# Kernel tuning notes

Measured on AMD Instinct MI355X. Metric: run time of the kernel, lower is better.

The kernel has to match this reference:

```python
import jax, jax.numpy as jnp
import numpy as np

EMBED_DIM = 256; N_HEADS = 8; HEAD_DIM = 32; N_PAIRS = 16
POS_DIM = 2; N_LEVELS = 4; NBH = [3, 5, 7, 9]
N_Q = 2048; BATCH = 2; FULL = 128
SPATIAL_THETA = 100.0; LEVEL_THETA = 10.0
LN_EPS = 1e-5


def _grids():
    offs, lvls = [], []
    for l, s in enumerate(NBH):
        ax = np.arange(s)
        g = np.stack(np.meshgrid(ax, ax, indexing='ij'), -1).reshape(-1, 2)
        offs.append(g - (s - 1) // 2)
        lvls.append(np.full(s * s, l))
    return (np.concatenate(offs).astype(np.int32), np.concatenate(lvls).astype(np.int32))

OFFSETS, LEVEL_IDS = _grids()  # [164,2], [164]
K_PER_Q = OFFSETS.shape[0]


def _apply_rope(x, pos, freqs):
    # x: [..., n_heads, n_pairs, 2]; pos: [..., 3]; freqs: [3, n_pairs]
    ang = pos @ freqs                      # [..., n_pairs]
    c = jnp.cos(ang)[..., None, :]         # broadcast over heads
    s = jnp.sin(ang)[..., None, :]
    x1, x2 = x[..., 0], x[..., 1]
    return jnp.stack([x1 * c - x2 * s, x1 * s + x2 * c], axis=-1)


def setup_inputs() -> dict:
    key = jax.random.key(0)
    ks = jax.random.split(key, 8)
    scale = EMBED_DIM ** -0.5
    i = jnp.arange(N_PAIRS, dtype=jnp.float32) / N_PAIRS
    rope_freqs = jnp.stack([SPATIAL_THETA ** -i, SPATIAL_THETA ** -i, LEVEL_THETA ** -i])  # [3,16]
    level_spatial_shapes = jnp.array([[FULL >> l, FULL >> l] for l in range(N_LEVELS)], jnp.int32)
    return {
        'query': jax.random.normal(ks[0], (N_Q, EMBED_DIM), jnp.float32),
        'query_spatial_positions': jax.random.uniform(ks[1], (N_Q, POS_DIM), jnp.float32) * (FULL - 1),
        'stacked_feature_maps': jax.random.normal(ks[2], (BATCH, N_LEVELS, FULL, FULL, EMBED_DIM), jnp.float32) * 0.02,
        'norm_w': jnp.ones((EMBED_DIM,), jnp.float32),
        'norm_b': jnp.zeros((EMBED_DIM,), jnp.float32),
        'q_w': jax.random.normal(ks[3], (EMBED_DIM, EMBED_DIM), jnp.float32) * scale,
        'k_w': jax.random.normal(ks[4], (EMBED_DIM, EMBED_DIM), jnp.float32) * scale,
        'v_w': jax.random.normal(ks[5], (EMBED_DIM, EMBED_DIM), jnp.float32) * scale,
        'out_w': jax.random.normal(ks[6], (EMBED_DIM, EMBED_DIM), jnp.float32) * scale,
        'rope_freqs': rope_freqs,
        'query_batch_offsets': jnp.array([0, N_Q // 2, N_Q], jnp.int32),
        'level_spatial_shapes': level_spatial_shapes,
    }


def reference(query, query_spatial_positions, stacked_feature_maps, norm_w, norm_b,
              q_w, k_w, v_w, out_w, rope_freqs, query_batch_offsets, level_spatial_shapes):
    n_q = query.shape[0]
    residual = query

    # pre-LayerNorm
    mu = query.mean(-1, keepdims=True)
    var = query.var(-1, keepdims=True)
    x = (query - mu) * jax.lax.rsqrt(var + LN_EPS) * norm_w + norm_b

    # query projection + RoPE (spatial dims + level dim; queries sit at max-res level 0)
    q = x @ q_w
    qpos = jnp.concatenate([query_spatial_positions, jnp.zeros((n_q, 1), query.dtype)], -1)  # [n_q,3]
    q_rot = _apply_rope(q.reshape(n_q, N_HEADS, N_PAIRS, 2), qpos, rope_freqs).reshape(n_q, N_HEADS, HEAD_DIM)

    # multilevel neighborhood indices
    shapes_f = level_spatial_shapes.astype(query.dtype)               # [L,2]
    scaling = shapes_f / shapes_f.max(0)                              # [L,2]
    scaled = query_spatial_positions[:, None, :] * scaling[None]      # [n_q,L,2]
    centers = jnp.floor(scaled).astype(jnp.int32)                     # [n_q,L,2]
    lvl = jnp.asarray(LEVEL_IDS)                                      # [K]
    idx = centers[:, lvl, :] + jnp.asarray(OFFSETS)[None]             # [n_q,K,2]
    lsh = level_spatial_shapes[lvl]                                   # [K,2]
    valid = jnp.all((idx >= 0) & (idx < lsh[None]), -1)               # [n_q,K]
    idxc = jnp.clip(idx, 0, lsh[None] - 1)

    # per-query batch ids from offsets
    b = jnp.searchsorted(query_batch_offsets, jnp.arange(n_q, dtype=query_batch_offsets.dtype), side='right') - 1

    # sparse gather of key/value features (unspecified -> zero)
    feats = stacked_feature_maps[b[:, None], lvl[None, :], idxc[..., 0], idxc[..., 1]]  # [n_q,K,E]
    feats = feats * valid[..., None].astype(feats.dtype)

    k = feats @ k_w
    v = feats @ v_w

    # key positions at full scale + level coordinate
    stride = (shapes_f.max(0)[None] / shapes_f)[lvl]                  # [K,2]
    kpos_sp = (idx.astype(query.dtype) + 0.5) * stride[None]          # [n_q,K,2]
    kpos = jnp.concatenate([kpos_sp, jnp.broadcast_to(lvl.astype(query.dtype), (n_q, K_PER_Q))[..., None]], -1)
    k_rot = _apply_rope(k.reshape(n_q, K_PER_Q, N_HEADS, N_PAIRS, 2), kpos, rope_freqs)
    k_rot = k_rot.reshape(n_q, K_PER_Q, N_HEADS, HEAD_DIM)

    # attention over the 164 gathered keys per query
    logits = jnp.einsum('nhd,nkhd->nhk', q_rot, k_rot) / np.sqrt(HEAD_DIM)
    logits = jnp.where(valid[:, None, :], logits, jnp.asarray(-1e9, logits.dtype))
    attn = jax.nn.softmax(logits, axis=-1)
    out = jnp.einsum('nhk,nkhd->nhd', attn, v.reshape(n_q, K_PER_Q, N_HEADS, HEAD_DIM))
    out = out.reshape(n_q, EMBED_DIM) @ out_w
    return out + residual
```

## Files before the change

### kernel.cpp

```cpp
#include <hip/hip_runtime.h>
#include <hip/hip_bf16.h>

typedef unsigned short u16;
typedef short short8 __attribute__((ext_vector_type(8)));
typedef float f32x4 __attribute__((ext_vector_type(4)));

#define ROWS_PER_BATCH 21760
#define TOT_ROWS 43520
#define KV_BLOCKS (TOT_ROWS / 128)

__device__ __forceinline__ u16 f2bf(float f){
  unsigned u = __builtin_bit_cast(unsigned, f);
  u += 0x7FFFu + ((u >> 16) & 1u);
  return (u16)(u >> 16);
}
__device__ __forceinline__ float bf2f(u16 h){
  return __builtin_bit_cast(float, ((unsigned)h) << 16);
}
__device__ __forceinline__ float bflo(unsigned u){ return __builtin_bit_cast(float, u << 16); }
__device__ __forceinline__ float bfhi(unsigned u){ return __builtin_bit_cast(float, u & 0xFFFF0000u); }
__device__ __forceinline__ unsigned pk2bf(float a, float b){
  __hip_bfloat162 h = __float22bfloat162_rn(make_float2(a, b));
  union { __hip_bfloat162 h2; unsigned u; } cv; cv.h2 = h; return cv.u;
}

__global__ __launch_bounds__(256) void prep_kernel(
    const float* __restrict__ qw, const float* __restrict__ kw,
    const float* __restrict__ vw, const float* __restrict__ ow,
    const float* __restrict__ q, const float* __restrict__ nw,
    const float* __restrict__ nb,
    u16* __restrict__ wtq, u16* __restrict__ wtk,
    u16* __restrict__ wtv, u16* __restrict__ wto, u16* __restrict__ x){
  const int bx = blockIdx.x;
  const int t = threadIdx.x;
  if (bx < 128){
    int e = bx * 256 + t;
    int which = e >> 13;
    int r = e & 8191;
    int cg = r >> 9;
    int kk = (r >> 6) & 7;
    int lane = r & 63;
    int quad = lane >> 4, mn = lane & 15;
    const float* s = which == 0 ? qw : which == 1 ? kw : which == 2 ? vw : ow;
    u16* d       = which == 0 ? wtq : which == 1 ? wtk : which == 2 ? wtv : wto;
    const float* base = s + (kk * 32 + quad * 8) * 256 + cg * 16 + mn;
    float e8[8];
    #pragma unroll
    for (int j = 0; j < 8; ++j) e8[j] = base[j * 256];
    uint4 o = { pk2bf(e8[0], e8[1]), pk2bf(e8[2], e8[3]),
                pk2bf(e8[4], e8[5]), pk2bf(e8[6], e8[7]) };
    *(uint4*)(d + (size_t)r * 8) = o;
  } else {
    const int row = (bx - 128) * 4 + (t >> 6);
    const int lane = t & 63;
    const float4 v = *(const float4*)(q + (size_t)row * 256 + lane * 4);
    float s1 = v.x + v.y + v.z + v.w;
    float s2 = v.x*v.x + v.y*v.y + v.z*v.z + v.w*v.w;
    #pragma unroll
    for (int o = 32; o > 0; o >>= 1){
      s1 += __shfl_xor(s1, o);
      s2 += __shfl_xor(s2, o);
    }
    float mu = s1 * (1.0f / 256.0f);
    float var = s2 * (1.0f / 256.0f) - mu * mu;
    float rs = rsqrtf(var + 1e-5f);
    const float4 wv = *(const float4*)(nw + lane * 4);
    const float4 bv = *(const float4*)(nb + lane * 4);
    float o0 = (v.x - mu) * rs * wv.x + bv.x;
    float o1 = (v.y - mu) * rs * wv.y + bv.y;
    float o2 = (v.z - mu) * rs * wv.z + bv.z;
    float o3 = (v.w - mu) * rs * wv.w + bv.w;
    uint2 pk = { pk2bf(o0, o1), pk2bf(o2, o3) };
    *(uint2*)(x + (size_t)row * 256 + lane * 4) = pk;
  }
}

__global__ __launch_bounds__(512, 4) void kv_qproj(const float* __restrict__ fm,
        const u16* __restrict__ wtkp, const u16* __restrict__ wtvp,
        const u16* __restrict__ wtqp, const u16* __restrict__ xbf,
        const float* __restrict__ rope,
        u16* __restrict__ krot, u16* __restrict__ vmap,
        float* __restrict__ qraw){
  __shared__ u16 bstage[32 * 512];
  __shared__ float slab[8][16][66];
  __shared__ unsigned sh_cs[8][16][16];

  const int t = threadIdx.x;

  if (blockIdx.x >= KV_BLOCKS){
    const int ob = (blockIdx.x - KV_BLOCKS) * 2 + (t >> 8);
    const int bx = ob & 127, by = ob >> 7;
    const int tt = t & 255;
    const int wv = tt >> 6;
    const int lane = tt & 63;
    const int mn = lane & 15;
    const int quad = lane >> 4;
    const int cg = by * 4 + wv;
    const int row0 = bx * 16;

    short8 af[8];
    {
      const u16* arow = xbf + (size_t)(row0 + mn) * 256 + quad * 8;
      #pragma unroll
      for (int kk = 0; kk < 8; ++kk)
        af[kk] = *(const short8*)(arow + kk * 32);
    }
    const u16* wb = wtqp + (size_t)((cg * 8) * 64 + lane) * 8;
    short8 bc = *(const short8*)wb;
    f32x4 acc = (f32x4){0.f, 0.f, 0.f, 0.f};
    #pragma unroll
    for (int kk = 0; kk < 8; ++kk){
      short8 bn;
      if (kk < 7) bn = *(const short8*)(wb + (size_t)(kk + 1) * 64 * 8);
      acc = __builtin_amdgcn_mfma_f32_16x16x32_bf16(af[kk], bc, acc, 0, 0, 0);
      bc = bn;
    }
    const int col = cg * 16 + mn;
    #pragma unroll
    for (int r = 0; r < 4; ++r)
      qraw[(size_t)(row0 + quad * 4 + r) * 256 + col] = acc[r];
    return;
  }

  const int w = t >> 6;
  const int lane = t & 63;
  const int row0 = blockIdx.x * 128 + w * 16;

  const int b = row0 / ROWS_PER_BATCH;
  const int rr = row0 - b * ROWS_PER_BATCH;
  int l, loff;
  if (rr < 16384)      { l = 0; loff = 0; }
  else if (rr < 20480) { l = 1; loff = 16384; }
  else if (rr < 21504) { l = 2; loff = 20480; }
  else                 { l = 3; loff = 21504; }
  const int logW = 7 - l;
  const int Wm1 = (128 >> l) - 1;
  const int cell0 = rr - loff;
  const float* fmbase = fm + (size_t)(b * 4 + l) * (128 * 128 * 256);

  const int mn = lane & 15;
  const int quad = lane >> 4;

  short8 af[8];
  {
    int cell = cell0 + mn;
    int y = cell >> logW, x = cell & Wm1;
    const float* arow = fmbase + (((y << 7) + x) << 8) + quad * 8;
    #pragma unroll
    for (int kk = 0; kk < 8; ++kk){
      float4 a0 = *(const float4*)(arow + kk * 32);
      float4 a1 = *(const float4*)(arow + kk * 32 + 4);
      union { short8 s; uint4 u; } cv;
      cv.u = (uint4){ pk2bf(a0.x, a0.y), pk2bf(a0.z, a0.w),
                      pk2bf(a1.x, a1.y), pk2bf(a1.z, a1.w) };
      af[kk] = cv.s;
    }
  }

  #pragma unroll
  for (int i = 0; i < 4; ++i){
    int id = i * 64 + lane;
    int lr = id >> 4, p = id & 15;
    int cell = cell0 + lr;
    int i0 = cell >> logW;
    int i1 = cell & Wm1;
    float fs = (float)(1 << l);
    float kx = ((float)i0 + 0.5f) * fs;
    float ky = ((float)i1 + 0.5f) * fs;
    float ang = kx * rope[p] + ky * rope[16 + p] + (float)l * rope[32 + p];
    sh_cs[w][lr][p] = pk2bf(__cosf(ang), __sinf(ang));
  }

  for (int m = 0; m < 2; ++m){
    const u16* wtp = m ? wtvp : wtkp;
    u16* outp = m ? vmap : krot;
    for (int cs2 = 0; cs2 < 4; ++cs2){
      __syncthreads();
      const u16* src = wtp + (size_t)cs2 * 16384;
      #pragma unroll
      for (int i = 0; i < 4; ++i)
        *(uint4*)(bstage + ((size_t)(i * 512 + t)) * 8) =
            *(const uint4*)(src + ((size_t)(i * 512 + t)) * 8);
      __syncthreads();

      f32x4 acc[4];
      #pragma unroll
      for (int i = 0; i < 4; ++i) acc[i] = (f32x4){0.f, 0.f, 0.f, 0.f};
      #pragma unroll
      for (int kk = 0; kk < 8; ++kk){
        #pragma unroll
        for (int tl = 0; tl < 4; ++tl){
          short8 bc = *(const short8*)(bstage + ((tl * 8 + kk) * 64 + lane) * 8);
          acc[tl] = __builtin_amdgcn_mfma_f32_16x16x32_bf16(af[kk], bc, acc[tl], 0, 0, 0);
        }
      }

      #pragma unroll
      for (int tl = 0; tl < 4; ++tl)
        #pragma unroll
        for (int r = 0; r < 4; ++r)
          slab[w][quad * 4 + r][tl * 16 + mn] = acc[tl][r];
      #pragma unroll
      for (int i = 0; i < 8; ++i){
        int pi = i * 64 + lane;
        int row = pi >> 5;
        int pl = pi & 31;
        float2 kv2 = *(const float2*)&slab[w][row][pl * 2];
        unsigned o;
        if (m == 0){
          unsigned csn = sh_cs[w][row][pl & 15];
          float c = bflo(csn), s = bfhi(csn);
          o = pk2bf(kv2.x * c - kv2.y * s, kv2.x * s + kv2.y * c);
        } else {
          o = pk2bf(kv2.x, kv2.y);
        }
        *(unsigned*)(outp + (size_t)(row0 + row) * 256 + cs2 * 64 + pl * 2) = o;
      }
    }
  }
}

__global__ __launch_bounds__(256) void gemm_xw(const u16* __restrict__ A,
        const u16* __restrict__ wt, const float* __restrict__ resid,
        float* __restrict__ out){
  const int t = threadIdx.x;
  const int row0 = blockIdx.x * 16;
  const int wv = t >> 6;
  const int lane = t & 63;
  const int mn = lane & 15;
  const int quad = lane >> 4;
  const int cg = blockIdx.y * 4 + wv;

  short8 af[8];
  {
    const u16* arow = A + (size_t)(row0 + mn) * 256 + quad * 8;
    #pragma unroll
    for (int kk = 0; kk < 8; ++kk)
      af[kk] = *(const short8*)(arow + kk * 32);
  }
  const u16* wb = wt + (size_t)((cg * 8) * 64 + lane) * 8;
  short8 bc = *(const short8*)wb;
  f32x4 acc = (f32x4){0.f, 0.f, 0.f, 0.f};
  #pragma unroll
  for (int kk = 0; kk < 8; ++kk){
    short8 bn;
    if (kk < 7) bn = *(const short8*)(wb + (size_t)(kk + 1) * 64 * 8);
    acc = __builtin_amdgcn_mfma_f32_16x16x32_bf16(af[kk], bc, acc, 0, 0, 0);
    bc = bn;
  }
  const int col = cg * 16 + mn;
  #pragma unroll
  for (int r = 0; r < 4; ++r){
    int row = row0 + quad * 4 + r;
    float val = acc[r];
    if (resid) val += resid[(size_t)row * 256 + col];
    out[(size_t)row * 256 + col] = val;
  }
}

__global__ __launch_bounds__(256) void attn3(
    const float* __restrict__ qraw, const float* __restrict__ qsp,
    const float* __restrict__ rope, const int* __restrict__ qbo, int nbo,
    const u16* __restrict__ krot, const u16* __restrict__ vmap,
    u16* __restrict__ ao){
  __shared__ float sh_q[4][8][33];
  __shared__ float sh_lg[4][168][8];
  __shared__ int   sh_row[4][168];
  __shared__ float sh_inv[4][8];
  const int t = threadIdx.x;
  const int w = t >> 6;
  const int lane = t & 63;
  const int qi = blockIdx.x * 4 + w;

  int bidx = 0;
  for (int j = 1; j < nbo; ++j) if (qi >= qbo[j]) bidx = j;
  const float p0 = qsp[qi * 2 + 0];
  const float p1 = qsp[qi * 2 + 1];

  #pragma unroll
  for (int it = 0; it < 4; ++it){
    int d = it * 64 + lane;
    float qv = qraw[(size_t)qi * 256 + d];
    int p = (d & 31) >> 1;
    float ang = p0 * rope[p] + p1 * rope[16 + p];
    float c = __cosf(ang), s = __sinf(ang);
    float partner = __shfl_xor(qv, 1);
    float val = (d & 1) ? (partner * s + qv * c) : (qv * c - partner * s);
    sh_q[w][d >> 5][d & 31] = val * 0.17677669529663687f;
  }

  #pragma unroll
  for (int it = 0; it < 3; ++it){
    int kk = it * 64 + lane;
    if (kk < 164){
      int l, dy, dx, loff;
      if (kk < 9)       { l = 0; int j = kk;      dy = j / 3 - 1; dx = j % 3 - 1; loff = 0; }
      else if (kk < 34) { l = 1; int j = kk - 9;  dy = j / 5 - 2; dx = j % 5 - 2; loff = 16384; }
      else if (kk < 83) { l = 2; int j = kk - 34; dy = j / 7 - 3; dx = j % 7 - 3; loff = 20480; }
      else              { l = 3; int j = kk - 83; dy = j / 9 - 4; dx = j % 9 - 4; loff = 21504; }
      float sc = 1.0f / (float)(1 << l);
      int i0 = (int)floorf(p0 * sc) + dy;
      int i1 = (int)floorf(p1 * sc) + dx;
      int W = 128 >> l;
      sh_row[w][kk] = (i0 < 0 || i0 >= W || i1 < 0 || i1 >= W)
                ? -1 : bidx * ROWS_PER_BATCH + loff + (i0 << (7 - l)) + i1;
    }
  }

  const int h = lane & 7;
  const int ksub = lane >> 3;
  float qreg[32];
  #pragma unroll
  for (int j = 0; j < 32; ++j) qreg[j] = sh_q[w][h][j];
  for (int pass = 0; pass < 21; ++pass){
    int kk = pass * 8 + ksub;
    if (kk < 164){
      int row = sh_row[w][kk];
      float lg = -1e9f;
      if (row >= 0){
        const uint4* kp = (const uint4*)(krot + (size_t)row * 256 + h * 32);
        uint4 A0 = kp[0], A1 = kp[1], A2 = kp[2], A3 = kp[3];
        unsigned uu[16];
        uu[0]=A0.x; uu[1]=A0.y; uu[2]=A0.z; uu[3]=A0.w;
        uu[4]=A1.x; uu[5]=A1.y; uu[6]=A1.z; uu[7]=A1.w;
        uu[8]=A2.x; uu[9]=A2.y; uu[10]=A2.z; uu[11]=A2.w;
        uu[12]=A3.x; uu[13]=A3.y; uu[14]=A3.z; uu[15]=A3.w;
        float s0 = 0.f, s1 = 0.f, s2 = 0.f, s3 = 0.f;
        #pragma unroll
        for (int j = 0; j < 4; ++j){
          s0 += qreg[2*j]      * bflo(uu[j])      + qreg[2*j+1]  * bfhi(uu[j]);
          s1 += qreg[2*j+8]    * bflo(uu[j+4])    + qreg[2*j+9]  * bfhi(uu[j+4]);
          s2 += qreg[2*j+16]   * bflo(uu[j+8])    + qreg[2*j+17] * bfhi(uu[j+8]);
          s3 += qreg[2*j+24]   * bflo(uu[j+12])   + qreg[2*j+25] * bfhi(uu[j+12]);
        }
        lg = (s0 + s1) + (s2 + s3);
      }
      sh_lg[w][kk][h] = lg;
    }
  }

  float mx = -1e30f;
  for (int kk = ksub; kk < 164; kk += 8) mx = fmaxf(mx, sh_lg[w][kk][h]);
  #pragma unroll
  for (int o = 8; o < 64; o <<= 1) mx = fmaxf(mx, __shfl_xor(mx, o));
  float ssum = 0.f;
  for (int kk = ksub; kk < 164; kk += 8){
    float e = __expf(sh_lg[w][kk][h] - mx);
    sh_lg[w][kk][h] = e;
    ssum += e;
  }
  #pragma unroll
  for (int o = 8; o < 64; o <<= 1) ssum += __shfl_xor(ssum, o);
  if (ksub == 0) sh_inv[w][h] = 1.0f / ssum;

  const int c = lane & 31;
  const int p2 = lane >> 5;
  const int hh = c >> 2;
  float a[8] = {0.f,0.f,0.f,0.f,0.f,0.f,0.f,0.f};
  #pragma unroll 4
  for (int ii = 0; ii < 82; ++ii){
    int kk = ii * 2 + p2;
    int row = sh_row[w][kk];
    int rc = row < 0 ? 0 : row;
    uint4 vv = *(const uint4*)(vmap + (size_t)rc * 256 + c * 8);
    float e = sh_lg[w][kk][hh];
    a[0] += e * bflo(vv.x); a[1] += e * bfhi(vv.x);
    a[2] += e * bflo(vv.y); a[3] += e * bfhi(vv.y);
    a[4] += e * bflo(vv.z); a[5] += e * bfhi(vv.z);
    a[6] += e * bflo(vv.w); a[7] += e * bfhi(vv.w);
  }
  #pragma unroll
  for (int j = 0; j < 8; ++j) a[j] += __shfl_xor(a[j], 32);
  if (p2 == 0){
    float inv = sh_inv[w][hh];
    uint4 o = { pk2bf(a[0]*inv, a[1]*inv), pk2bf(a[2]*inv, a[3]*inv),
                pk2bf(a[4]*inv, a[5]*inv), pk2bf(a[6]*inv, a[7]*inv) };
    *(uint4*)(ao + (size_t)qi * 256 + c * 8) = o;
  }
}

extern "C" void kernel_launch(void* const* d_in, const int* in_sizes, int n_in,
                              void* d_out, int out_size, void* d_ws, size_t ws_size,
                              hipStream_t stream) {
  (void)n_in; (void)out_size; (void)ws_size;
  const float* query  = (const float*)d_in[0];
  const float* qsp    = (const float*)d_in[1];
  const float* fm     = (const float*)d_in[2];
  const float* norm_w = (const float*)d_in[3];
  const float* norm_b = (const float*)d_in[4];
  const float* q_w    = (const float*)d_in[5];
  const float* k_w    = (const float*)d_in[6];
  const float* v_w    = (const float*)d_in[7];
  const float* out_w  = (const float*)d_in[8];
  const float* rope   = (const float*)d_in[9];
  const int*   qbo    = (const int*)d_in[10];
  float* out = (float*)d_out;
  const int n_q = in_sizes[0] / 256;
  const int nbo = in_sizes[10];

  char* p = (char*)d_ws;
  u16* krot = (u16*)p;                       p += (size_t)TOT_ROWS * 256 * 2;
  u16* vmap = (u16*)p;                       p += (size_t)TOT_ROWS * 256 * 2;
  float* qraw = (float*)p;                   p += (size_t)n_q * 256 * 4;
  u16* xbf = (u16*)p;                        p += (size_t)n_q * 256 * 2;
  u16* wtq = (u16*)p;                        p += 65536 * 2;
  u16* wtk = (u16*)p;                        p += 65536 * 2;
  u16* wtv = (u16*)p;                        p += 65536 * 2;
  u16* wto = (u16*)p;
  u16* ao = xbf;

  hipLaunchKernelGGL(prep_kernel, dim3(128 + n_q / 4), dim3(256), 0, stream,
                     q_w, k_w, v_w, out_w, query, norm_w, norm_b,
                     wtq, wtk, wtv, wto, xbf);
  hipLaunchKernelGGL(kv_qproj, dim3(KV_BLOCKS + n_q / 8 / 2 * 2 / 2), dim3(512), 0, stream,
                     fm, wtk, wtv, wtq, xbf, rope, krot, vmap, qraw);
  hipLaunchKernelGGL(attn3, dim3(n_q / 4), dim3(256), 0, stream,
                     qraw, qsp, rope, qbo, nbo, krot, vmap, ao);
  hipLaunchKernelGGL(gemm_xw, dim3(n_q / 16, 4), dim3(256), 0, stream,
                     ao, wto, query, out);
}
```

Baseline: 252.6 us.

## Fuse output projection and residual into attention kernel, drop gemm launch

Removes the separate output-projection GEMM kernel. The attention kernel now stages each query's normalized head outputs in shared memory and multiplies them by a row-major bf16 out_w using scalar FMAs, then adds the residual. The Q-projection blocks in kv_qproj now each handle two tiles in a loop, which halves their count. This saves one launch and the bf16 round trip of the attention output, at the cost of a scalar (non-MFMA) 256x256 matvec per query that rereads the weight matrix from cache in every wave.

```diff
diff --git a/kernel.cpp b/kernel.cpp
--- a/kernel.cpp
+++ b/kernel.cpp
@@ -30,26 +30,35 @@
     const float* __restrict__ q, const float* __restrict__ nw,
     const float* __restrict__ nb,
     u16* __restrict__ wtq, u16* __restrict__ wtk,
-    u16* __restrict__ wtv, u16* __restrict__ wto, u16* __restrict__ x){
+    u16* __restrict__ wtv, u16* __restrict__ wtor, u16* __restrict__ x){
   const int bx = blockIdx.x;
   const int t = threadIdx.x;
   if (bx < 128){
     int e = bx * 256 + t;
     int which = e >> 13;
     int r = e & 8191;
-    int cg = r >> 9;
-    int kk = (r >> 6) & 7;
-    int lane = r & 63;
-    int quad = lane >> 4, mn = lane & 15;
-    const float* s = which == 0 ? qw : which == 1 ? kw : which == 2 ? vw : ow;
-    u16* d       = which == 0 ? wtq : which == 1 ? wtk : which == 2 ? wtv : wto;
-    const float* base = s + (kk * 32 + quad * 8) * 256 + cg * 16 + mn;
-    float e8[8];
-    #pragma unroll
-    for (int j = 0; j < 8; ++j) e8[j] = base[j * 256];
-    uint4 o = { pk2bf(e8[0], e8[1]), pk2bf(e8[2], e8[3]),
-                pk2bf(e8[4], e8[5]), pk2bf(e8[6], e8[7]) };
-    *(uint4*)(d + (size_t)r * 8) = o;
+    if (which == 3){
+      int e8 = r * 8;
+      float4 a0 = *(const float4*)(ow + e8);
+      float4 a1 = *(const float4*)(ow + e8 + 4);
+      uint4 o = { pk2bf(a0.x, a0.y), pk2bf(a0.z, a0.w),
+                  pk2bf(a1.x, a1.y), pk2bf(a1.z, a1.w) };
+      *(uint4*)(wtor + e8) = o;
+    } else {
+      int cg = r >> 9;
+      int kk = (r >> 6) & 7;
+      int lane = r & 63;
+      int quad = lane >> 4, mn = lane & 15;
+      const float* s = which == 0 ? qw : which == 1 ? kw : vw;
+      u16* d       = which == 0 ? wtq : which == 1 ? wtk : wtv;
+      const float* base = s + (kk * 32 + quad * 8) * 256 + cg * 16 + mn;
+      float e8[8];
+      #pragma unroll
+      for (int j = 0; j < 8; ++j) e8[j] = base[j * 256];
+      uint4 o = { pk2bf(e8[0], e8[1]), pk2bf(e8[2], e8[3]),
+                  pk2bf(e8[4], e8[5]), pk2bf(e8[6], e8[7]) };
+      *(uint4*)(d + (size_t)r * 8) = o;
+    }
   } else {
     const int row = (bx - 128) * 4 + (t >> 6);
     const int lane = t & 63;
@@ -88,37 +97,40 @@
   const int t = threadIdx.x;
 
   if (blockIdx.x >= KV_BLOCKS){
-    const int ob = (blockIdx.x - KV_BLOCKS) * 2 + (t >> 8);
-    const int bx = ob & 127, by = ob >> 7;
-    const int tt = t & 255;
-    const int wv = tt >> 6;
-    const int lane = tt & 63;
-    const int mn = lane & 15;
-    const int quad = lane >> 4;
-    const int cg = by * 4 + wv;
-    const int row0 = bx * 16;
-
-    short8 af[8];
-    {
-      const u16* arow = xbf + (size_t)(row0 + mn) * 256 + quad * 8;
-      #pragma unroll
-      for (int kk = 0; kk < 8; ++kk)
-        af[kk] = *(const short8*)(arow + kk * 32);
-    }
-    const u16* wb = wtqp + (size_t)((cg * 8) * 64 + lane) * 8;
-    short8 bc = *(const short8*)wb;
-    f32x4 acc = (f32x4){0.f, 0.f, 0.f, 0.f};
-    #pragma unroll
-    for (int kk = 0; kk < 8; ++kk){
-      short8 bn;
-      if (kk < 7) bn = *(const short8*)(wb + (size_t)(kk + 1) * 64 * 8);
-      acc = __builtin_amdgcn_mfma_f32_16x16x32_bf16(af[kk], bc, acc, 0, 0, 0);
-      bc = bn;
-    }
-    const int col = cg * 16 + mn;
-    #pragma unroll
-    for (int r = 0; r < 4; ++r)
-      qraw[(size_t)(row0 + quad * 4 + r) * 256 + col] = acc[r];
+    #pragma unroll 1
+    for (int step = 0; step < 2; ++step){
+      const int ob = (blockIdx.x - KV_BLOCKS) * 4 + step * 2 + (t >> 8);
+      const int bx = ob & 127, by = ob >> 7;
+      const int tt = t & 255;
+      const int wv = tt >> 6;
+      const int lane = tt & 63;
+      const int mn = lane & 15;
+      const int quad = lane >> 4;
+      const int cg = by * 4 + wv;
+      const int row0 = bx * 16;
+
+      short8 af[8];
+      {
+        const u16* arow = xbf + (size_t)(row0 + mn) * 256 + quad * 8;
+        #pragma unroll
+        for (int kk = 0; kk < 8; ++kk)
+          af[kk] = *(const short8*)(arow + kk * 32);
+      }
+      const u16* wb = wtqp + (size_t)((cg * 8) * 64 + lane) * 8;
+      short8 bc = *(const short8*)wb;
+      f32x4 acc = (f32x4){0.f, 0.f, 0.f, 0.f};
+      #pragma unroll
+      for (int kk = 0; kk < 8; ++kk){
+        short8 bn;
+        if (kk < 7) bn = *(const short8*)(wb + (size_t)(kk + 1) * 64 * 8);
+        acc = __builtin_amdgcn_mfma_f32_16x16x32_bf16(af[kk], bc, acc, 0, 0, 0);
+        bc = bn;
+      }
+      const int col = cg * 16 + mn;
+      #pragma unroll
+      for (int r = 0; r < 4; ++r)
+        qraw[(size_t)(row0 + quad * 4 + r) * 256 + col] = acc[r];
+    }
     return;
   }
 
@@ -220,53 +232,17 @@
   }
 }
 
-__global__ __launch_bounds__(256) void gemm_xw(const u16* __restrict__ A,
-        const u16* __restrict__ wt, const float* __restrict__ resid,
-        float* __restrict__ out){
-  const int t = threadIdx.x;
-  const int row0 = blockIdx.x * 16;
-  const int wv = t >> 6;
-  const int lane = t & 63;
-  const int mn = lane & 15;
-  const int quad = lane >> 4;
-  const int cg = blockIdx.y * 4 + wv;
-
-  short8 af[8];
-  {
-    const u16* arow = A + (size_t)(row0 + mn) * 256 + quad * 8;
-    #pragma unroll
-    for (int kk = 0; kk < 8; ++kk)
-      af[kk] = *(const short8*)(arow + kk * 32);
-  }
-  const u16* wb = wt + (size_t)((cg * 8) * 64 + lane) * 8;
-  short8 bc = *(const short8*)wb;
-  f32x4 acc = (f32x4){0.f, 0.f, 0.f, 0.f};
-  #pragma unroll
-  for (int kk = 0; kk < 8; ++kk){
-    short8 bn;
-    if (kk < 7) bn = *(const short8*)(wb + (size_t)(kk + 1) * 64 * 8);
-    acc = __builtin_amdgcn_mfma_f32_16x16x32_bf16(af[kk], bc, acc, 0, 0, 0);
-    bc = bn;
-  }
-  const int col = cg * 16 + mn;
-  #pragma unroll
-  for (int r = 0; r < 4; ++r){
-    int row = row0 + quad * 4 + r;
-    float val = acc[r];
-    if (resid) val += resid[(size_t)row * 256 + col];
-    out[(size_t)row * 256 + col] = val;
-  }
-}
-
 __global__ __launch_bounds__(256) void attn3(
     const float* __restrict__ qraw, const float* __restrict__ qsp,
     const float* __restrict__ rope, const int* __restrict__ qbo, int nbo,
     const u16* __restrict__ krot, const u16* __restrict__ vmap,
-    u16* __restrict__ ao){
+    const u16* __restrict__ wtor, const float* __restrict__ resid,
+    float* __restrict__ out){
   __shared__ float sh_q[4][8][33];
   __shared__ float sh_lg[4][168][8];
   __shared__ int   sh_row[4][168];
   __shared__ float sh_inv[4][8];
+  __shared__ float sh_o[4][256];
   const int t = threadIdx.x;
   const int w = t >> 6;
   const int lane = t & 63;
@@ -373,9 +349,33 @@
   for (int j = 0; j < 8; ++j) a[j] += __shfl_xor(a[j], 32);
   if (p2 == 0){
     float inv = sh_inv[w][hh];
-    uint4 o = { pk2bf(a[0]*inv, a[1]*inv), pk2bf(a[2]*inv, a[3]*inv),
-                pk2bf(a[4]*inv, a[5]*inv), pk2bf(a[6]*inv, a[7]*inv) };
-    *(uint4*)(ao + (size_t)qi * 256 + c * 8) = o;
+    #pragma unroll
+    for (int j = 0; j < 8; ++j) sh_o[w][c * 8 + j] = a[j] * inv;
+  }
+
+  {
+    const int kpar = lane >> 5;
+    float b2[8] = {0.f,0.f,0.f,0.f,0.f,0.f,0.f,0.f};
+    #pragma unroll 4
+    for (int ii = 0; ii < 128; ++ii){
+      int k = ii * 2 + kpar;
+      float ak = sh_o[w][k];
+      uint4 ww = *(const uint4*)(wtor + (size_t)k * 256 + c * 8);
+      b2[0] += ak * bflo(ww.x); b2[1] += ak * bfhi(ww.x);
+      b2[2] += ak * bflo(ww.y); b2[3] += ak * bfhi(ww.y);
+      b2[4] += ak * bflo(ww.z); b2[5] += ak * bfhi(ww.z);
+      b2[6] += ak * bflo(ww.w); b2[7] += ak * bfhi(ww.w);
+    }
+    #pragma unroll
+    for (int j = 0; j < 8; ++j) b2[j] += __shfl_xor(b2[j], 32);
+    if (kpar == 0){
+      const float* rp = resid + (size_t)qi * 256 + c * 8;
+      float4 r0 = *(const float4*)rp;
+      float4 r1 = *(const float4*)(rp + 4);
+      float* op = out + (size_t)qi * 256 + c * 8;
+      *(float4*)op       = (float4){b2[0]+r0.x, b2[1]+r0.y, b2[2]+r0.z, b2[3]+r0.w};
+      *(float4*)(op + 4) = (float4){b2[4]+r1.x, b2[5]+r1.y, b2[6]+r1.z, b2[7]+r1.w};
+    }
   }
 }
 
@@ -406,16 +406,13 @@
   u16* wtq = (u16*)p;                        p += 65536 * 2;
   u16* wtk = (u16*)p;                        p += 65536 * 2;
   u16* wtv = (u16*)p;                        p += 65536 * 2;
-  u16* wto = (u16*)p;
-  u16* ao = xbf;
+  u16* wtor = (u16*)p;
 
   hipLaunchKernelGGL(prep_kernel, dim3(128 + n_q / 4), dim3(256), 0, stream,
                      q_w, k_w, v_w, out_w, query, norm_w, norm_b,
-                     wtq, wtk, wtv, wto, xbf);
-  hipLaunchKernelGGL(kv_qproj, dim3(KV_BLOCKS + n_q / 8 / 2 * 2 / 2), dim3(512), 0, stream,
+                     wtq, wtk, wtv, wtor, xbf);
+  hipLaunchKernelGGL(kv_qproj, dim3(KV_BLOCKS + n_q / 16), dim3(512), 0, stream,
                      fm, wtk, wtv, wtq, xbf, rope, krot, vmap, qraw);
   hipLaunchKernelGGL(attn3, dim3(n_q / 4), dim3(256), 0, stream,
-                     qraw, qsp, rope, qbo, nbo, krot, vmap, ao);
-  hipLaunchKernelGGL(gemm_xw, dim3(n_q / 16, 4), dim3(256), 0, stream,
-                     ao, wto, query, out);
-}
+                     qraw, qsp, rope, qbo, nbo, krot, vmap, wtor, query, out);
+}
```

Result: slower. 259.9 us (+2.9%).
